# Performance work log

Hardware: AMD Instinct MI355X
Metric: run time of the kernel (lower is better)

## Reference

```python
import jax, jax.numpy as jnp
import numpy as np

N = 100000   # nodes
E = 800000   # edges (avg degree 8)
IN = 128     # in_dim
H = 128      # hidden_dim
L = 3        # num_layers
EPS = 1e-5   # torch LayerNorm default


def setup_inputs() -> dict:
    key = jax.random.key(0)
    ks = jax.random.split(key, 10)
    s = 0.05
    # DAG edge list: src < dst guarantees acyclicity and node N-1 is a sink.
    rng = np.random.default_rng(0)
    src = rng.integers(0, N - 1, size=E)
    dst = src + 1 + (rng.random(E) * (N - 1 - src)).astype(np.int64)
    return {
        "node_feats": jax.random.normal(ks[0], (N, IN), jnp.float32),
        "src": jnp.asarray(src, jnp.int32),
        "dst": jnp.asarray(dst, jnp.int32),
        "W_in": jax.random.normal(ks[1], (IN, H), jnp.float32) * s,
        "b_in": jnp.zeros((H,), jnp.float32),
        "Ws": jax.random.normal(ks[2], (L, H, H), jnp.float32) * s,
        "bs": jnp.zeros((L, H), jnp.float32),
        "Wn": jax.random.normal(ks[3], (L, H, H), jnp.float32) * s,
        "bn": jnp.zeros((L, H), jnp.float32),
        "Wg": jax.random.normal(ks[4], (L, 2 * H, H), jnp.float32) * s,
        "bg": jnp.zeros((L, H), jnp.float32),
        "gamma": jnp.ones((L, H), jnp.float32),
        "beta": jnp.zeros((L, H), jnp.float32),
        "W_att": jax.random.normal(ks[5], (H, H), jnp.float32) * s,
        "b_att": jnp.zeros((H,), jnp.float32),
        "W_score": jax.random.normal(ks[6], (H, 1), jnp.float32) * s,
        "b_score": jnp.zeros((1,), jnp.float32),
    }


def reference(node_feats, src, dst, W_in, b_in, Ws, bs, Wn, bn, Wg, bg,
              gamma, beta, W_att, b_att, W_score, b_score):
    n = node_feats.shape[0]
    ones_e = jnp.ones(src.shape, node_feats.dtype)
    indeg = jax.ops.segment_sum(ones_e, dst, num_segments=n)          # [N]
    has_pred = (indeg > 0).astype(node_feats.dtype)[:, None]          # [N,1]
    inv_deg = (1.0 / jnp.maximum(indeg, 1.0))[:, None]                # [N,1]
    outdeg = jax.ops.segment_sum(ones_e, src, num_segments=n)
    sink_mask = outdeg == 0                                           # [N]

    h = node_feats @ W_in + b_in                                      # [N,H]
    for i in range(Ws.shape[0]):
        hs = h @ Ws[i] + bs[i]
        # predecessor mean of layer-input h (no within-layer recurrence)
        neigh = jax.ops.segment_sum(h[src], dst, num_segments=n) * inv_deg
        hn = neigh @ Wn[i] + bn[i]
        m = hs + has_pred * hn  # nodes with no preds use m = hs only (bias too)
        gate = jax.nn.sigmoid(jnp.concatenate([h, m], axis=-1) @ Wg[i] + bg[i])
        v = gate * m + (1.0 - gate) * h
        mu = v.mean(-1, keepdims=True)
        var = ((v - mu) ** 2).mean(-1, keepdims=True)
        v = (v - mu) * jax.lax.rsqrt(var + EPS) * gamma[i] + beta[i]
        h = jax.nn.relu(v)

    # attention pooling over sink nodes only
    a = jnp.tanh(h @ W_att + b_att)
    scores = (a @ W_score)[:, 0] + b_score[0]
    scores = jnp.where(sink_mask, scores, -jnp.inf)
    w = jax.nn.softmax(scores, axis=0)  # zero weight on non-sinks
    graph_emb = (w[:, None] * h).sum(0)
    return h, graph_emb
```

## Files before the change

### kernel.cpp

```cpp
#include <hip/hip_runtime.h>
#include <cmath>

typedef unsigned short u16;
typedef unsigned int   u32;
typedef __attribute__((ext_vector_type(8))) short bf16x8;
typedef __attribute__((ext_vector_type(4))) float f32x4;
typedef __attribute__((ext_vector_type(4))) u32   u32x4;

__device__ __forceinline__ float bf2f(u16 u){
    union { u32 i; float f; } x; x.i = ((u32)u) << 16; return x.f;
}
__device__ __forceinline__ u16 f2bf(float f){
    union { float f; u32 i; } x; x.f = f;
    u32 r = x.i + 0x7fffu + ((x.i >> 16) & 1u);
    return (u16)(r >> 16);
}

__device__ __forceinline__ size_t frag_idx(int n, int k){
    int t = n >> 4, sl = n & 15, kk = k >> 5, g16 = (k >> 3) & 3, e = k & 7;
    return ((size_t)(t*4 + kk)*64 + g16*16 + sl)*8 + e;
}


__global__ void k_count(const int* __restrict__ src, const int* __restrict__ dst,
                        int* cnt, int* notsink, int* pos, int E){
    int e = blockIdx.x*256 + threadIdx.x;
    if (e < E){
        pos[e] = atomicAdd(&cnt[dst[e]], 1);
        notsink[src[e]] = 1;
    }
}

__global__ void k_scan1(const int* __restrict__ in, int* blocksum, int N){
    __shared__ int sh[256];
    int tid = threadIdx.x;
    int base = blockIdx.x*1024 + tid*4;
    int s = 0;
    for (int j=0;j<4;j++){ int i = base+j; s += (i < N) ? in[i] : 0; }
    sh[tid] = s; __syncthreads();
    for (int d=128; d>0; d>>=1){ if (tid < d) sh[tid] += sh[tid+d]; __syncthreads(); }
    if (tid == 0) blocksum[blockIdx.x] = sh[0];
}

__global__ void k_scan2(int* blocksum, int nb){
    if (threadIdx.x == 0){
        int run = 0;
        for (int i=0;i<nb;i++){ int v = blocksum[i]; blocksum[i] = run; run += v; }
    }
}

__global__ void k_scan3(const int* __restrict__ in, const int* __restrict__ blockoff,
                        const int* __restrict__ notsink,
                        int* out, float* inv_deg, float* haspred,
                        int* sink_list, int* nsink, int N){
    __shared__ int sh[256];
    int tid = threadIdx.x;
    int base = blockIdx.x*1024 + tid*4;
    int e[4]; int s = 0;
    for (int j=0;j<4;j++){ int i = base+j; e[j] = (i < N) ? in[i] : 0; s += e[j]; }
    sh[tid] = s; __syncthreads();
    for (int d=1; d<256; d<<=1){
        int t = (tid >= d) ? sh[tid-d] : 0;
        __syncthreads();
        sh[tid] += t;
        __syncthreads();
    }
    int excl = sh[tid] - s + blockoff[blockIdx.x];
    for (int j=0;j<4;j++){
        int i = base+j;
        if (i < N){
            out[i] = excl; excl += e[j];
            inv_deg[i] = 1.0f / (float)(e[j] > 1 ? e[j] : 1);
            haspred[i] = e[j] > 0 ? 1.0f : 0.0f;
            if (notsink[i] == 0){
                int p = atomicAdd(nsink, 1);
                sink_list[p] = i;
            }
        }
    }
}

__global__ void k_place(const int* __restrict__ src, const int* __restrict__ dst,
                        const int* __restrict__ row_ptr, const int* __restrict__ pos,
                        int* csr_src, int E){
    int e = blockIdx.x*256 + threadIdx.x;
    if (e < E)
        csr_src[row_ptr[dst[e]] + pos[e]] = src[e];
}

__global__ void k_wt_plain(const float* __restrict__ W_in, const float* __restrict__ W_att,
                           const float* __restrict__ Ws, const float* __restrict__ Wn,
                           u16* WT_in, u16* WT_att, u16* WB){
    int i = blockIdx.x*256 + threadIdx.x;
    if (i < 32768){
        const float* srcm = (i < 16384) ? W_in : W_att;
        u16* dstm = (i < 16384) ? WT_in : WT_att;
        int w = i & 16383, n = w >> 7, k = w & 127;
        dstm[n*128 + k] = f2bf(srcm[k*128 + n]);
    } else {
        int off = i - 32768;
        int m  = off / 49152;
        int w  = off % 49152;
        int l  = w >> 14, ww = w & 16383;
        int n  = ww >> 7, k = ww & 127;
        const float* srcm = m ? Wn : Ws;
        u16* dstm = WB + ((size_t)l*2 + m)*32768;
        dstm[frag_idx(n, k)] = f2bf(srcm[(size_t)l*16384 + k*128 + n]);
    }
}

__global__ void k_wt_comp(const float* __restrict__ Ws, const float* __restrict__ Wn,
                          const float* __restrict__ Wg,
                          const float* __restrict__ bs, const float* __restrict__ bn,
                          u16* WB, float* vb){
    __shared__ float cols[2][128];
    int l = blockIdx.x / 129;
    int b = blockIdx.x % 129;
    const float* Wgb = Wg + (size_t)l*32768 + 16384;
    int tid = threadIdx.x;
    if (b == 128){
        int n = tid & 127;
        const float* bv = (tid < 128) ? (bs + l*128) : (bn + l*128);
        float acc = 0.f;
        for (int j=0;j<128;j++) acc += bv[j] * Wgb[j*128 + n];
        vb[l*256 + (tid>>7)*128 + n] = acc;
        return;
    }
    int m  = b >> 6;
    int n0 = (b & 63) * 2;
    int nn = tid >> 7, k = tid & 127;
    cols[tid>>7][tid&127] = Wgb[(size_t)(tid&127)*128 + n0 + (tid>>7)];
    __syncthreads();
    const float* A = (m ? Wn : Ws) + (size_t)l*16384;
    float acc = 0.f;
    for (int j=0;j<128;j++) acc += A[k*128 + j] * cols[nn][j];
    int n = n0 + nn;
    if (m == 0) acc += Wg[(size_t)l*32768 + k*128 + n];
    u16* dstm = WB + ((size_t)l*2 + m)*32768;
    dstm[frag_idx(128 + n, k)] = f2bf(acc);
}


__global__ void k_neigh(const u16* __restrict__ h, const int* __restrict__ row_ptr,
                        const int* __restrict__ indeg, const float* __restrict__ inv_deg,
                        const int* __restrict__ csr_src, u16* __restrict__ neigh, int N){
    int wid  = (blockIdx.x*256 + threadIdx.x) >> 6;
    int lane = threadIdx.x & 63;
    int sub = lane >> 4, sl = lane & 15;
    int node = wid*4 + sub;
    bool valid = node < N;
    int deg   = valid ? indeg[node]   : 0;
    int start = valid ? row_ptr[node] : 0;
    float acc[8] = {0.f,0.f,0.f,0.f,0.f,0.f,0.f,0.f};
    for (int e0 = 0; __any(e0 < deg); e0 += 16){
        int idx = 0;
        if (e0 + sl < deg) idx = csr_src[start + e0 + sl];
        int cnt = deg - e0;
        #pragma unroll
        for (int j = 0; j < 16; j++){
            int sidx = __shfl(idx, (sub << 4) | j);
            if (j < cnt){
                bf16x8 v = *(const bf16x8*)(h + (size_t)sidx*128 + sl*8);
                #pragma unroll
                for (int t=0;t<8;t++) acc[t] += bf2f((u16)v[t]);
            }
        }
    }
    if (valid){
        float iv = inv_deg[node];
        u16 o[8];
        #pragma unroll
        for (int t=0;t<8;t++) o[t] = f2bf(acc[t]*iv);
        *(u32x4*)(neigh + (size_t)node*128 + sl*8) = *(const u32x4*)o;
    }
}


__device__ __forceinline__ void stage_A_f32(const float* __restrict__ A, u16 (*lA)[136],
                                            int row0, int n_rows, int tid){
    #pragma unroll
    for (int i=0;i<4;i++){
        int c = i*256 + tid;
        int r = c >> 4, col8 = (c & 15) * 8;
        u16 o[8] = {0,0,0,0,0,0,0,0};
        if (row0 + r < n_rows){
            float4 v0 = *(const float4*)(A + (size_t)(row0 + r)*128 + col8);
            float4 v1 = *(const float4*)(A + (size_t)(row0 + r)*128 + col8 + 4);
            o[0]=f2bf(v0.x); o[1]=f2bf(v0.y); o[2]=f2bf(v0.z); o[3]=f2bf(v0.w);
            o[4]=f2bf(v1.x); o[5]=f2bf(v1.y); o[6]=f2bf(v1.z); o[7]=f2bf(v1.w);
        }
        *(u32x4*)&lA[r][col8] = *(const u32x4*)o;
    }
}

__device__ __forceinline__ void stage_B(const u16* __restrict__ BT, int Ks, int koff0,
                                        u16 (*lB)[136], int tid){
    #pragma unroll
    for (int i=0;i<8;i++){
        int c = i*256 + tid;
        int n = c >> 4, col8 = (c & 15) * 8;
        u32x4 v = *(const u32x4*)(BT + (size_t)n*Ks + koff0 + col8);
        *(u32x4*)&lB[n][col8] = v;
    }
}

__device__ __forceinline__ void mfma_tile(const u16 (*lA)[136], const u16 (*lB)[136],
                                          int wave, int lane, f32x4* acc){
    #pragma unroll
    for (int kk=0;kk<4;kk++){
        int koff = kk*32 + (lane >> 4) * 8;
        bf16x8 a = *(const bf16x8*)&lA[wave*16 + (lane & 15)][koff];
        #pragma unroll
        for (int t=0;t<8;t++){
            bf16x8 b = *(const bf16x8*)&lB[t*16 + (lane & 15)][koff];
            acc[t] = __builtin_amdgcn_mfma_f32_16x16x32_bf16(a, b, acc[t], 0, 0, 0);
        }
    }
}


__global__ __launch_bounds__(256) void k_gemm_in(
    const float* __restrict__ A, const u16* __restrict__ BT,
    const float* __restrict__ bias, u16* __restrict__ C, int n_rows)
{
    __shared__ u16 lA[64][136];
    __shared__ u16 lB[128][136];
    int tid = threadIdx.x, wave = tid >> 6, lane = tid & 63;
    int row0 = blockIdx.x * 64;
    f32x4 acc[8];
    #pragma unroll
    for (int t=0;t<8;t++) acc[t] = (f32x4){0.f,0.f,0.f,0.f};
    stage_A_f32(A, lA, row0, n_rows, tid);
    stage_B(BT, 128, 0, lB, tid);
    __syncthreads();
    mfma_tile(lA, lB, wave, lane, acc);

    int sl = lane & 15;
    int rbase = wave*16 + (lane >> 4)*4;
    float bc[8];
    #pragma unroll
    for (int t=0;t<8;t++) bc[t] = bias[t*16 + sl];
    for (int r=0;r<4;r++){
        int row = row0 + rbase + r;
        if (row >= n_rows) continue;
        #pragma unroll
        for (int t=0;t<8;t++)
            C[(size_t)row*128 + t*16 + sl] = f2bf(acc[t][r] + bc[t]);
    }
}


__global__ __launch_bounds__(256, 3) void k_layer(
    const u16* __restrict__ H, const u16* __restrict__ Ng,
    const u16* __restrict__ WB,
    const float* __restrict__ bs, const float* __restrict__ bn,
    const float* __restrict__ bg,
    const float* __restrict__ vb1, const float* __restrict__ vb2,
    const float* __restrict__ gamma, const float* __restrict__ beta,
    const float* __restrict__ haspred,
    u16* __restrict__ Hb, float* __restrict__ Hf, int n_rows)
{
    __shared__ u16 lH[64][132];
    __shared__ u16 lB[2][8192];
    int tid = threadIdx.x, wave = tid >> 6, lane = tid & 63;
    int sl = lane & 15, g16 = lane >> 4;
    int row0 = blockIdx.x * 64;

    int arow = row0 + wave*16 + sl;
    bool av = arow < n_rows;
    bf16x8 a1[4], a2[4];
    #pragma unroll
    for (int kk=0;kk<4;kk++){
        a1[kk] = (bf16x8){0,0,0,0,0,0,0,0};
        a2[kk] = (bf16x8){0,0,0,0,0,0,0,0};
    }
    if (av){
        #pragma unroll
        for (int kk=0;kk<4;kk++){
            a1[kk] = *(const bf16x8*)(H  + (size_t)arow*128 + kk*32 + g16*8);
            a2[kk] = *(const bf16x8*)(Ng + (size_t)arow*128 + kk*32 + g16*8);
        }
    }

    #pragma unroll
    for (int i=0;i<4;i++){
        int c = i*256 + tid;
        int r = c >> 4, col8 = (c & 15) * 8;
        u32x4 v = {0,0,0,0};
        if (row0 + r < n_rows)
            v = *(const u32x4*)(H + (size_t)(row0 + r)*128 + col8);
        *(u32x4*)&lH[r][col8] = v;
    }

    u32x4 st[4];
    #pragma unroll
    for (int i=0;i<4;i++)
        st[i] = *(const u32x4*)(WB + (size_t)(i*256 + tid)*8);
    #pragma unroll
    for (int i=0;i<4;i++)
        *(u32x4*)&lB[0][(i*256 + tid)*8] = st[i];

    f32x4 acc[16];
    #pragma unroll
    for (int t=0;t<16;t++) acc[t] = (f32x4){0.f,0.f,0.f,0.f};
    __syncthreads();

    #pragma unroll
    for (int s=0;s<8;s++){
        int cur = s & 1;
        if (s < 7){
            const u16* sp = WB + (size_t)(s+1)*8192;
            #pragma unroll
            for (int i=0;i<4;i++)
                st[i] = *(const u32x4*)(sp + (size_t)(i*256 + tid)*8);
        }
        const u16* bp = &lB[cur][lane*8];
        #pragma unroll
        for (int j=0;j<4;j++){
            #pragma unroll
            for (int kk=0;kk<4;kk++){
                bf16x8 b = *(const bf16x8*)(bp + ((j*4 + kk) << 9));
                int ai = (s & 3)*4 + j;
                acc[ai] = __builtin_amdgcn_mfma_f32_16x16x32_bf16(
                    (s >= 4) ? a2[kk] : a1[kk], b, acc[ai], 0, 0, 0);
            }
        }
        if (s < 7){
            #pragma unroll
            for (int i=0;i<4;i++)
                *(u32x4*)&lB[cur ^ 1][(i*256 + tid)*8] = st[i];
        }
        __syncthreads();
    }

    int rbase = wave*16 + g16*4;
    float bM[8], bnl[8], bG[8], vb2l[8], gam[8], bet[8];
    #pragma unroll
    for (int t=0;t<8;t++){
        int c = t*16 + sl;
        bM[t] = bs[c]; bnl[t] = bn[c];
        bG[t] = bg[c] + vb1[c]; vb2l[t] = vb2[c];
        gam[t] = gamma[c]; bet[t] = beta[c];
    }
    if (Hf){
        for (int r=0;r<4;r++){
            int row = row0 + rbase + r;
            if (row >= n_rows) continue;
            float hp = haspred[row];
            float v[8], s = 0.f;
            #pragma unroll
            for (int t=0;t<8;t++){
                int c = t*16 + sl;
                float m = acc[t][r]   + bM[t] + hp*bnl[t];
                float x = acc[t+8][r] + bG[t] + hp*vb2l[t];
                float gg = 1.f/(1.f + expf(-x));
                float hv = bf2f(lH[rbase + r][c]);
                v[t] = gg*m + (1.f - gg)*hv;
                s += v[t];
            }
            s += __shfl_xor(s,1); s += __shfl_xor(s,2); s += __shfl_xor(s,4); s += __shfl_xor(s,8);
            float mu = s * (1.f/128.f);
            float q = 0.f;
            #pragma unroll
            for (int t=0;t<8;t++){ float d = v[t]-mu; q += d*d; }
            q += __shfl_xor(q,1); q += __shfl_xor(q,2); q += __shfl_xor(q,4); q += __shfl_xor(q,8);
            float rs = rsqrtf(q*(1.f/128.f) + 1e-5f);
            #pragma unroll
            for (int t=0;t<8;t++){
                float o = (v[t]-mu)*rs*gam[t] + bet[t];
                Hf[(size_t)row*128 + t*16 + sl] = o > 0.f ? o : 0.f;
            }
        }
    } else {
        float ov[4][8];
        for (int r=0;r<4;r++){
            int row = row0 + rbase + r;
            float hp = (row < n_rows) ? haspred[row] : 0.f;
            float v[8], s = 0.f;
            #pragma unroll
            for (int t=0;t<8;t++){
                int c = t*16 + sl;
                float m = acc[t][r]   + bM[t] + hp*bnl[t];
                float x = acc[t+8][r] + bG[t] + hp*vb2l[t];
                float gg = 1.f/(1.f + expf(-x));
                float hv = bf2f(lH[rbase + r][c]);
                v[t] = gg*m + (1.f - gg)*hv;
                s += v[t];
            }
            s += __shfl_xor(s,1); s += __shfl_xor(s,2); s += __shfl_xor(s,4); s += __shfl_xor(s,8);
            float mu = s * (1.f/128.f);
            float q = 0.f;
            #pragma unroll
            for (int t=0;t<8;t++){ float d = v[t]-mu; q += d*d; }
            q += __shfl_xor(q,1); q += __shfl_xor(q,2); q += __shfl_xor(q,4); q += __shfl_xor(q,8);
            float rs = rsqrtf(q*(1.f/128.f) + 1e-5f);
            #pragma unroll
            for (int t=0;t<8;t++){
                float o = (v[t]-mu)*rs*gam[t] + bet[t];
                ov[r][t] = o > 0.f ? o : 0.f;
            }
        }
        __syncthreads();
        #pragma unroll
        for (int r=0;r<4;r++)
            #pragma unroll
            for (int t=0;t<8;t++)
                lH[rbase + r][t*16 + sl] = f2bf(ov[r][t]);
        __syncthreads();
        #pragma unroll
        for (int i=0;i<4;i++){
            int c = i*256 + tid;
            int r = c >> 4, col8 = (c & 15) * 8;
            if (row0 + r < n_rows)
                *(u32x4*)&Hb[(size_t)(row0 + r)*128 + col8] = *(const u32x4*)&lH[r][col8];
        }
    }
}


__global__ __launch_bounds__(256) void k_att_sink(
    const float* __restrict__ Hf, const u16* __restrict__ BT,
    const float* __restrict__ b_att, const float* __restrict__ Wsc,
    const float* __restrict__ bsc, const int* __restrict__ sink_list,
    const int* __restrict__ nsink, float* __restrict__ scores_sink)
{
    __shared__ u16 lA[64][136];
    __shared__ u16 lB[128][136];
    int ns = *nsink;
    int tid = threadIdx.x, wave = tid >> 6, lane = tid & 63;
    int sl = lane & 15;
    stage_B(BT, 128, 0, lB, tid);
    float bac[8], wc[8];
    #pragma unroll
    for (int t=0;t<8;t++){ bac[t] = b_att[t*16 + sl]; wc[t] = Wsc[t*16 + sl]; }
    float b0 = bsc[0];
    int rbase = wave*16 + (lane >> 4)*4;

    for (int c0 = blockIdx.x*64; c0 < ns; c0 += gridDim.x*64){
        __syncthreads();
        #pragma unroll
        for (int i=0;i<4;i++){
            int c = i*256 + tid;
            int r = c >> 4, col8 = (c & 15) * 8;
            u16 o[8] = {0,0,0,0,0,0,0,0};
            if (c0 + r < ns){
                int row = sink_list[c0 + r];
                float4 v0 = *(const float4*)(Hf + (size_t)row*128 + col8);
                float4 v1 = *(const float4*)(Hf + (size_t)row*128 + col8 + 4);
                o[0]=f2bf(v0.x); o[1]=f2bf(v0.y); o[2]=f2bf(v0.z); o[3]=f2bf(v0.w);
                o[4]=f2bf(v1.x); o[5]=f2bf(v1.y); o[6]=f2bf(v1.z); o[7]=f2bf(v1.w);
            }
            *(u32x4*)&lA[r][col8] = *(const u32x4*)o;
        }
        __syncthreads();
        f32x4 acc[8];
        #pragma unroll
        for (int t=0;t<8;t++) acc[t] = (f32x4){0.f,0.f,0.f,0.f};
        mfma_tile(lA, lB, wave, lane, acc);

        for (int r=0;r<4;r++){
            int i = c0 + rbase + r;
            if (i >= ns) continue;
            float p = 0.f;
            #pragma unroll
            for (int t=0;t<8;t++) p += tanhf(acc[t][r] + bac[t]) * wc[t];
            p += __shfl_xor(p,1); p += __shfl_xor(p,2); p += __shfl_xor(p,4); p += __shfl_xor(p,8);
            if (sl == 0)
                scores_sink[i] = p + b0;
        }
    }
}


__global__ void k_pool_sink(const float* __restrict__ Hf, const int* __restrict__ sink_list,
                            const int* __restrict__ nsink,
                            const float* __restrict__ scores_sink,
                            float* __restrict__ out){
    __shared__ float sh[256];
    __shared__ float swg[2];
    int ns = *nsink;
    int tid = threadIdx.x;
    int col = tid & 127, grp = tid >> 7;
    float acc = 0.f, wsum = 0.f;
    for (int i = grp; i < ns; i += 2){
        float w = expf(scores_sink[i]);
        acc += w * Hf[(size_t)sink_list[i]*128 + col];
        if (col == 0) wsum += w;
    }
    sh[tid] = acc;
    if (col == 0) swg[grp] = wsum;
    __syncthreads();
    if (tid < 128) out[tid] = (sh[tid] + sh[tid+128]) / (swg[0] + swg[1]);
}


extern "C" void kernel_launch(void* const* d_in, const int* in_sizes, int n_in,
                              void* d_out, int out_size, void* d_ws, size_t ws_size,
                              hipStream_t stream)
{
    const float* node_feats = (const float*)d_in[0];
    const int* src     = (const int*)d_in[1];
    const int* dst     = (const int*)d_in[2];
    const float* W_in    = (const float*)d_in[3];
    const float* b_in    = (const float*)d_in[4];
    const float* Ws      = (const float*)d_in[5];
    const float* bs      = (const float*)d_in[6];
    const float* Wn      = (const float*)d_in[7];
    const float* bn      = (const float*)d_in[8];
    const float* Wg      = (const float*)d_in[9];
    const float* bg      = (const float*)d_in[10];
    const float* gamma   = (const float*)d_in[11];
    const float* beta    = (const float*)d_in[12];
    const float* W_att   = (const float*)d_in[13];
    const float* b_att   = (const float*)d_in[14];
    const float* W_score = (const float*)d_in[15];
    const float* b_score = (const float*)d_in[16];

    const int N = in_sizes[0] / 128;
    const int E = in_sizes[1];

    char* w = (char*)d_ws;
    auto alloc = [&](size_t bytes)->char* {
        char* p = w; w += (bytes + 255) & ~(size_t)255; return p;
    };
    u16* WT_in  = (u16*)alloc(128*128*2);
    u16* WT_att = (u16*)alloc(128*128*2);
    u16* WB     = (u16*)alloc(3*2*256*128*2);
    float* vb   = (float*)alloc(3*256*4);
    int* cnt      = (int*)alloc((size_t)N*4);
    int* notsink  = (int*)alloc((size_t)N*4);
    int* nsink    = (int*)alloc(256);
    size_t zero_bytes = (size_t)((char*)nsink + 256 - (char*)cnt);
    int* pos      = (int*)alloc((size_t)E*4);
    int* row_ptr  = (int*)alloc((size_t)N*4);
    int* blocksum = (int*)alloc(1024*4);
    int* csr_src  = (int*)alloc((size_t)E*4);
    float* inv_deg = (float*)alloc((size_t)N*4);
    float* haspred = (float*)alloc((size_t)N*4);
    int* sink_list = (int*)alloc((size_t)N*4);
    float* scores_sink = (float*)alloc((size_t)N*4);
    u16* buf0 = (u16*)alloc((size_t)N*128*2);
    u16* buf1 = (u16*)alloc((size_t)N*128*2);
    u16* bufn = (u16*)alloc((size_t)N*128*2);

    float* h_out   = (float*)d_out;
    float* emb_out = h_out + (size_t)N*128;

    hipMemsetAsync(cnt, 0, zero_bytes, stream);

    k_wt_plain<<<512, 256, 0, stream>>>(W_in, W_att, Ws, Wn, WT_in, WT_att, WB);
    k_wt_comp<<<3*129, 256, 0, stream>>>(Ws, Wn, Wg, bs, bn, WB, vb);

    k_count<<<(E+255)/256, 256, 0, stream>>>(src, dst, cnt, notsink, pos, E);

    int nb = (N + 1023) / 1024;
    k_scan1<<<nb, 256, 0, stream>>>(cnt, blocksum, N);
    k_scan2<<<1, 256, 0, stream>>>(blocksum, nb);
    k_scan3<<<nb, 256, 0, stream>>>(cnt, blocksum, notsink, row_ptr, inv_deg, haspred,
                                    sink_list, nsink, N);
    k_place<<<(E+255)/256, 256, 0, stream>>>(src, dst, row_ptr, pos, csr_src, E);

    int gblk = (N + 63) / 64;
    int nblk = (N + 15) / 16;

    k_gemm_in<<<gblk, 256, 0, stream>>>(node_feats, WT_in, b_in, buf0, N);

    u16* hin = buf0;
    for (int i=0;i<3;i++){
        k_neigh<<<nblk, 256, 0, stream>>>(hin, row_ptr, cnt, inv_deg, csr_src, bufn, N);
        u16* hb  = (hin == buf0) ? buf1 : buf0;
        float* hf = (i == 2) ? h_out : nullptr;
        k_layer<<<gblk, 256, 0, stream>>>(hin, bufn,
                                          WB + (size_t)i*65536,
                                          bs + i*128, bn + i*128, bg + i*128,
                                          vb + i*256, vb + i*256 + 128,
                                          gamma + i*128, beta + i*128, haspred,
                                          hb, hf, N);
        hin = hb;
    }

    k_att_sink<<<8, 256, 0, stream>>>(h_out, WT_att, b_att, W_score, b_score,
                                      sink_list, nsink, scores_sink);
    k_pool_sink<<<1, 256, 0, stream>>>(h_out, sink_list, nsink, scores_sink, emb_out);

    (void)n_in; (void)out_size; (void)ws_size;
}
```

Measured before the change: 531.3 us.

## Fuse predecessor-mean gather into the layer GEMM kernel via shared memory

Removes the separate neighbor-aggregation kernel and computes each block's 64 rows of predecessor means inside k_layer, staging them in shared memory (aliased onto the second weight buffer) before loading them as MFMA A-fragments. This drops a kernel launch per layer and the write and re-read of an N x 128 bf16 intermediate. In exchange, the irregular gather now runs inside the GEMM block with its occupancy limits, and an extra barrier is added before the weight pipeline starts.

```diff
diff --git a/kernel.cpp b/kernel.cpp
--- a/kernel.cpp
+++ b/kernel.cpp
@@ -141,41 +141,6 @@
 }
 
 
-__global__ void k_neigh(const u16* __restrict__ h, const int* __restrict__ row_ptr,
-                        const int* __restrict__ indeg, const float* __restrict__ inv_deg,
-                        const int* __restrict__ csr_src, u16* __restrict__ neigh, int N){
-    int wid  = (blockIdx.x*256 + threadIdx.x) >> 6;
-    int lane = threadIdx.x & 63;
-    int sub = lane >> 4, sl = lane & 15;
-    int node = wid*4 + sub;
-    bool valid = node < N;
-    int deg   = valid ? indeg[node]   : 0;
-    int start = valid ? row_ptr[node] : 0;
-    float acc[8] = {0.f,0.f,0.f,0.f,0.f,0.f,0.f,0.f};
-    for (int e0 = 0; __any(e0 < deg); e0 += 16){
-        int idx = 0;
-        if (e0 + sl < deg) idx = csr_src[start + e0 + sl];
-        int cnt = deg - e0;
-        #pragma unroll
-        for (int j = 0; j < 16; j++){
-            int sidx = __shfl(idx, (sub << 4) | j);
-            if (j < cnt){
-                bf16x8 v = *(const bf16x8*)(h + (size_t)sidx*128 + sl*8);
-                #pragma unroll
-                for (int t=0;t<8;t++) acc[t] += bf2f((u16)v[t]);
-            }
-        }
-    }
-    if (valid){
-        float iv = inv_deg[node];
-        u16 o[8];
-        #pragma unroll
-        for (int t=0;t<8;t++) o[t] = f2bf(acc[t]*iv);
-        *(u32x4*)(neigh + (size_t)node*128 + sl*8) = *(const u32x4*)o;
-    }
-}
-
-
 __device__ __forceinline__ void stage_A_f32(const float* __restrict__ A, u16 (*lA)[136],
                                             int row0, int n_rows, int tid){
     #pragma unroll
@@ -251,8 +216,10 @@
 
 
 __global__ __launch_bounds__(256, 3) void k_layer(
-    const u16* __restrict__ H, const u16* __restrict__ Ng,
+    const u16* __restrict__ H,
     const u16* __restrict__ WB,
+    const int* __restrict__ row_ptr, const int* __restrict__ indeg,
+    const float* __restrict__ inv_deg, const int* __restrict__ csr_src,
     const float* __restrict__ bs, const float* __restrict__ bn,
     const float* __restrict__ bg,
     const float* __restrict__ vb1, const float* __restrict__ vb2,
@@ -261,26 +228,28 @@
     u16* __restrict__ Hb, float* __restrict__ Hf, int n_rows)
 {
     __shared__ u16 lH[64][132];
-    __shared__ u16 lB[2][8192];
+    __shared__ u16 lB0[8192];
+    __shared__ u16 lB1[8448];
+    u16 (*lN)[132] = (u16 (*)[132])lB1;
     int tid = threadIdx.x, wave = tid >> 6, lane = tid & 63;
     int sl = lane & 15, g16 = lane >> 4;
     int row0 = blockIdx.x * 64;
 
     int arow = row0 + wave*16 + sl;
     bool av = arow < n_rows;
-    bf16x8 a1[4], a2[4];
-    #pragma unroll
-    for (int kk=0;kk<4;kk++){
-        a1[kk] = (bf16x8){0,0,0,0,0,0,0,0};
-        a2[kk] = (bf16x8){0,0,0,0,0,0,0,0};
-    }
+    bf16x8 a1[4];
+    #pragma unroll
+    for (int kk=0;kk<4;kk++) a1[kk] = (bf16x8){0,0,0,0,0,0,0,0};
     if (av){
         #pragma unroll
-        for (int kk=0;kk<4;kk++){
-            a1[kk] = *(const bf16x8*)(H  + (size_t)arow*128 + kk*32 + g16*8);
-            a2[kk] = *(const bf16x8*)(Ng + (size_t)arow*128 + kk*32 + g16*8);
-        }
-    }
+        for (int kk=0;kk<4;kk++)
+            a1[kk] = *(const bf16x8*)(H + (size_t)arow*128 + kk*32 + g16*8);
+    }
+
+    u32x4 st[4];
+    #pragma unroll
+    for (int i=0;i<4;i++)
+        st[i] = *(const u32x4*)(WB + (size_t)(i*256 + tid)*8);
 
     #pragma unroll
     for (int i=0;i<4;i++){
@@ -292,29 +261,61 @@
         *(u32x4*)&lH[r][col8] = v;
     }
 
-    u32x4 st[4];
-    #pragma unroll
-    for (int i=0;i<4;i++)
-        st[i] = *(const u32x4*)(WB + (size_t)(i*256 + tid)*8);
-    #pragma unroll
-    for (int i=0;i<4;i++)
-        *(u32x4*)&lB[0][(i*256 + tid)*8] = st[i];
+    {
+        int sub = lane >> 4;
+        for (int q=0;q<4;q++){
+            int nrow = wave*16 + q*4 + sub;
+            int node = row0 + nrow;
+            bool valid = node < n_rows;
+            int deg   = valid ? indeg[node]   : 0;
+            int start = valid ? row_ptr[node] : 0;
+            float iv  = valid ? inv_deg[node] : 0.f;
+            float ga[8] = {0.f,0.f,0.f,0.f,0.f,0.f,0.f,0.f};
+            for (int e0 = 0; __any(e0 < deg); e0 += 16){
+                int idx = 0;
+                if (e0 + sl < deg) idx = csr_src[start + e0 + sl];
+                int cnt = deg - e0;
+                #pragma unroll
+                for (int j = 0; j < 16; j++){
+                    int sidx = __shfl(idx, (sub << 4) | j);
+                    if (j < cnt){
+                        bf16x8 v = *(const bf16x8*)(H + (size_t)sidx*128 + sl*8);
+                        #pragma unroll
+                        for (int t=0;t<8;t++) ga[t] += bf2f((u16)v[t]);
+                    }
+                }
+            }
+            u16 o[8];
+            #pragma unroll
+            for (int t=0;t<8;t++) o[t] = f2bf(ga[t]*iv);
+            *(u32x4*)&lN[nrow][sl*8] = *(const u32x4*)o;
+        }
+    }
 
     f32x4 acc[16];
     #pragma unroll
     for (int t=0;t<16;t++) acc[t] = (f32x4){0.f,0.f,0.f,0.f};
     __syncthreads();
 
+    bf16x8 a2[4];
+    #pragma unroll
+    for (int kk=0;kk<4;kk++)
+        a2[kk] = *(const bf16x8*)&lN[wave*16 + sl][kk*32 + g16*8];
+
+    #pragma unroll
+    for (int i=0;i<4;i++)
+        *(u32x4*)&lB0[(i*256 + tid)*8] = st[i];
+    __syncthreads();
+
     #pragma unroll
     for (int s=0;s<8;s++){
-        int cur = s & 1;
         if (s < 7){
             const u16* sp = WB + (size_t)(s+1)*8192;
             #pragma unroll
             for (int i=0;i<4;i++)
                 st[i] = *(const u32x4*)(sp + (size_t)(i*256 + tid)*8);
         }
-        const u16* bp = &lB[cur][lane*8];
+        const u16* bp = ((s & 1) ? lB1 : lB0) + lane*8;
         #pragma unroll
         for (int j=0;j<4;j++){
             #pragma unroll
@@ -326,9 +327,10 @@
             }
         }
         if (s < 7){
+            u16* wp = (s & 1) ? lB0 : lB1;
             #pragma unroll
             for (int i=0;i<4;i++)
-                *(u32x4*)&lB[cur ^ 1][(i*256 + tid)*8] = st[i];
+                *(u32x4*)&wp[(i*256 + tid)*8] = st[i];
         }
         __syncthreads();
     }
@@ -541,7 +543,6 @@
     float* scores_sink = (float*)alloc((size_t)N*4);
     u16* buf0 = (u16*)alloc((size_t)N*128*2);
     u16* buf1 = (u16*)alloc((size_t)N*128*2);
-    u16* bufn = (u16*)alloc((size_t)N*128*2);
 
     float* h_out   = (float*)d_out;
     float* emb_out = h_out + (size_t)N*128;
@@ -561,17 +562,16 @@
     k_place<<<(E+255)/256, 256, 0, stream>>>(src, dst, row_ptr, pos, csr_src, E);
 
     int gblk = (N + 63) / 64;
-    int nblk = (N + 15) / 16;
 
     k_gemm_in<<<gblk, 256, 0, stream>>>(node_feats, WT_in, b_in, buf0, N);
 
     u16* hin = buf0;
     for (int i=0;i<3;i++){
-        k_neigh<<<nblk, 256, 0, stream>>>(hin, row_ptr, cnt, inv_deg, csr_src, bufn, N);
         u16* hb  = (hin == buf0) ? buf1 : buf0;
         float* hf = (i == 2) ? h_out : nullptr;
-        k_layer<<<gblk, 256, 0, stream>>>(hin, bufn,
+        k_layer<<<gblk, 256, 0, stream>>>(hin,
                                           WB + (size_t)i*65536,
+                                          row_ptr, cnt, inv_deg, csr_src,
                                           bs + i*128, bn + i*128, bg + i*128,
                                           vb + i*256, vb + i*256 + 128,
                                           gamma + i*128, beta + i*128, haspred,
```

New measurement: 794.1 us. +49.5%, slower.
